# Performance work log

Measured on AMD Instinct MI355X. Metric: run time of the kernel, lower is better.

The kernel has to match this reference:

```python
import jax, jax.numpy as jnp
import numpy as np

B, NV, RN, SN = 1, 4, 1024, 128
H = W = 256
C_FEAT = 32   # img_feat_dim
D_VIEW = 32   # view transformer d_model
PE_D = 8      # PE_d_hid
D_RAY = D_VIEW + PE_D  # 40
NHEAD = 8
EPS_LN = 1e-5


def _layernorm(x, g, b):
    m = x.mean(-1, keepdims=True)
    v = ((x - m) ** 2).mean(-1, keepdims=True)
    return (x - m) * jax.lax.rsqrt(v + EPS_LN) * g + b


def _linear_attention(q, k, v):
    # LoFTR kernelized linear attention; q,k,v: (n, L, h, d)
    Q = jax.nn.elu(q) + 1.0
    K = jax.nn.elu(k) + 1.0
    L = v.shape[1]
    KV = jnp.einsum('nshd,nshv->nhdv', K, v / L)
    Z = 1.0 / (jnp.einsum('nlhd,nhd->nlh', Q, K.sum(axis=1)) + 1e-6)
    return jnp.einsum('nlhd,nhdv,nlh->nlhv', Q, KV, Z) * L


def _loftr_self_layer(x, Wq, Wk, Wv, Wm, g1, b1, W1, W2, g2, b2):
    # LoFTREncoderLayer with self-attention (x is both query and source)
    n, L, d = x.shape
    dim = d // NHEAD
    q = (x @ Wq).reshape(n, L, NHEAD, dim)
    k = (x @ Wk).reshape(n, L, NHEAD, dim)
    v = (x @ Wv).reshape(n, L, NHEAD, dim)
    msg = _linear_attention(q, k, v).reshape(n, L, d) @ Wm
    msg = _layernorm(msg, g1, b1)
    msg = jax.nn.relu(jnp.concatenate([x, msg], -1) @ W1) @ W2
    msg = _layernorm(msg, g2, b2)
    return x + msg


def _grid_sample_2d(img, pix):
    # img: (N,C,H,W); pix: (N,RN,SN,2) in pixel coords.
    # bilinear, align_corners=True, zero padding; mask = in-bounds.
    N, C, Hh, Ww = img.shape
    x, y = pix[..., 0], pix[..., 1]
    mask = ((x >= 0) & (x <= Ww - 1) & (y >= 0) & (y <= Hh - 1)).astype(img.dtype)
    x0 = jnp.floor(x)
    y0 = jnp.floor(y)
    flat = img.reshape(N, C, Hh * Ww)

    def gather(ix, iy):
        valid = ((ix >= 0) & (ix < Ww) & (iy >= 0) & (iy < Hh)).astype(img.dtype)
        idx = (jnp.clip(iy, 0, Hh - 1) * Ww + jnp.clip(ix, 0, Ww - 1)).astype(jnp.int32)
        out = jnp.take_along_axis(flat, idx.reshape(N, 1, -1), axis=2)
        return out.reshape(N, C, ix.shape[1], ix.shape[2]) * valid[:, None]

    wx1 = x - x0
    wy1 = y - y0
    out = (gather(x0, y0) * ((1 - wx1) * (1 - wy1))[:, None]
           + gather(x0 + 1, y0) * (wx1 * (1 - wy1))[:, None]
           + gather(x0, y0 + 1) * ((1 - wx1) * wy1)[:, None]
           + gather(x0 + 1, y0 + 1) * (wx1 * wy1)[:, None])
    return out, mask


def _order_posenc(d_hid, n):
    pos = np.arange(n)[:, None].astype(np.float64)
    j = np.arange(d_hid)[None, :]
    tab = pos / np.power(10000.0, 2 * (j // 2) / d_hid)
    tab[:, 0::2] = np.sin(tab[:, 0::2])
    tab[:, 1::2] = np.cos(tab[:, 1::2])
    return jnp.asarray(tab, dtype=jnp.float32)


def _forward(point3D, source_imgs, source_imgs_feat, ref_pose_inv, source_poses_inv,
             source_poses, view_token,
             vt_Wq, vt_Wk, vt_Wv, vt_Wm, vt_g1, vt_b1, vt_W1, vt_W2, vt_g2, vt_b2,
             rt_Wq, rt_Wk, rt_Wv, rt_Wm, rt_g1, rt_b1, rt_W1, rt_W2, rt_g2, rt_b2,
             dm_W1, dm_b1, dm_W2, dm_b2, dm_W3, dm_b3,
             rw_W1, rw_b1, rw_W2, rw_b2, rw_W3, rw_b3):
    b, nv, _, h, w = source_imgs.shape
    _, rn, sn, _ = point3D.shape

    # relative viewing directions (B,NV,RN,SN,3)
    v1 = point3D - ref_pose_inv[:, None, None, :3, -1]
    v2 = point3D[:, None] - source_poses_inv[:, :, None, None, :3, -1]
    v1 = v1 / jnp.linalg.norm(v1, axis=-1, keepdims=True)
    v2 = v2 / jnp.linalg.norm(v2, axis=-1, keepdims=True)
    dir_relative = v1[:, None] - v2

    # project points into all source views: (B,NV,3,RN,SN)
    pts_h = jnp.concatenate([point3D, jnp.ones_like(point3D[..., :1])], -1)
    pip = jnp.einsum('bnij,brsj->bnirs', source_poses, pts_h)[:, :, :3]
    mask_valid_depth = (pip[:, :, 2] > 0).astype(point3D.dtype)
    pix = pip[:, :, :2] / pip[:, :, 2:3]
    grid = jnp.moveaxis(pix, 2, -1).reshape(b * nv, rn, sn, 2)

    feat_s, mask = _grid_sample_2d(source_imgs_feat.reshape(b * nv, -1, h, w), grid)
    rgb_s, _ = _grid_sample_2d(source_imgs.reshape(b * nv, -1, h, w), grid)
    mask = mask.reshape(b, nv, rn, sn) * mask_valid_depth

    # per-point multi-view tokens: (B*RN*SN, NV, C)
    x = feat_s.reshape(b, nv, -1, rn, sn).transpose(0, 3, 4, 1, 2).reshape(b * rn * sn, nv, -1)
    tok = jnp.broadcast_to(view_token, (x.shape[0], 1, view_token.shape[-1]))
    x = jnp.concatenate([tok, x], axis=1)  # prepend view token -> L = NV+1
    x = _loftr_self_layer(x, vt_Wq, vt_Wk, vt_Wv, vt_Wm, vt_g1, vt_b1, vt_W1, vt_W2, vt_g2, vt_b2)

    x1 = jnp.moveaxis(x, 1, 0)          # (NV+1, B*RN*SN, C)
    view_feature = x1[1:]
    x = x1[0].reshape(b * rn, sn, -1)   # token output per sample along ray

    pe = _order_posenc(PE_D, sn)        # (SN, 8)
    x = jnp.concatenate([x, jnp.broadcast_to(pe, (b * rn, sn, PE_D))], -1)
    x = _loftr_self_layer(x, rt_Wq, rt_Wk, rt_Wv, rt_Wm, rt_g1, rt_b1, rt_W1, rt_W2, rt_g2, rt_b2)

    hdm = jax.nn.relu(x @ dm_W1 + dm_b1)
    hdm = jax.nn.relu(hdm @ dm_W2 + dm_b2)
    srdf = hdm @ dm_W3 + dm_b3           # (B*RN, SN, 1)

    # radiance blending weights over views
    vf = view_feature.reshape(nv, b, rn, sn, -1).transpose(1, 2, 3, 0, 4)  # (B,RN,SN,NV,C)
    dr = dir_relative.transpose(0, 2, 3, 1, 4)                             # (B,RN,SN,NV,3)
    xw = jnp.concatenate([vf, dr], -1)
    xw = jax.nn.relu(xw @ rw_W1 + rw_b1)
    xw = jax.nn.relu(xw @ rw_W2 + rw_b2)
    xw = xw @ rw_W3 + rw_b3                                                # (B,RN,SN,NV,1)
    m = mask.transpose(0, 2, 3, 1)[..., None]
    xw = jnp.where(m == 0, -1e9, xw)
    weight = jax.nn.softmax(xw, axis=-2)
    w_bn = weight[..., 0].transpose(0, 3, 1, 2)[:, :, None]                # (B,NV,1,RN,SN)
    radiance = (rgb_s.reshape(b, nv, 3, rn, sn) * w_bn).sum(axis=1)        # (B,3,RN,SN)
    radiance = radiance.transpose(0, 2, 3, 1).reshape(b * rn * sn, 3)
    return radiance, srdf, pip


def setup_inputs() -> dict:
    key = jax.random.key(0)
    ks = jax.random.split(key, 4)
    u = jax.random.uniform(ks[0], (B, RN, SN, 3), dtype=jnp.float32)
    point3D = jnp.concatenate([u[..., :2] - 0.5, u[..., 2:] + 1.0], -1)  # x,y in [-.5,.5], z in [1,2]
    source_imgs = jax.random.normal(ks[1], (B, NV, 3, H, W), dtype=jnp.float32) * 0.5
    source_imgs_feat = jax.random.normal(ks[2], (B, NV, C_FEAT, H, W), dtype=jnp.float32) * 0.5

    f = 200.0
    P = np.array([[f, 0, W / 2, 0], [0, f, H / 2, 0], [0, 0, 1, 0], [0, 0, 0, 1]], np.float32)
    source_poses = jnp.asarray(np.broadcast_to(P, (B, NV, 4, 4)).copy())
    ref_pose_inv = jnp.asarray(np.broadcast_to(np.eye(4, dtype=np.float32), (B, 4, 4)).copy())
    spi = np.broadcast_to(np.eye(4, dtype=np.float32), (B, NV, 4, 4)).copy()
    spi[:, :, 0, 3] = np.linspace(-0.2, 0.2, NV, dtype=np.float32)  # camera centers
    source_poses_inv = jnp.asarray(spi)

    pk = jax.random.split(ks[3], 20)

    def lin(k, i, o):
        return jax.random.normal(k, (i, o), dtype=jnp.float32) * 0.05

    d, dr = D_VIEW, D_RAY
    params = dict(
        view_token=jax.random.normal(pk[0], (1, d), dtype=jnp.float32),
        vt_Wq=lin(pk[1], d, d), vt_Wk=lin(pk[2], d, d), vt_Wv=lin(pk[3], d, d), vt_Wm=lin(pk[4], d, d),
        vt_g1=jnp.ones(d), vt_b1=jnp.zeros(d),
        vt_W1=lin(pk[5], 2 * d, 2 * d), vt_W2=lin(pk[6], 2 * d, d),
        vt_g2=jnp.ones(d), vt_b2=jnp.zeros(d),
        rt_Wq=lin(pk[7], dr, dr), rt_Wk=lin(pk[8], dr, dr), rt_Wv=lin(pk[9], dr, dr), rt_Wm=lin(pk[10], dr, dr),
        rt_g1=jnp.ones(dr), rt_b1=jnp.zeros(dr),
        rt_W1=lin(pk[11], 2 * dr, 2 * dr), rt_W2=lin(pk[12], 2 * dr, dr),
        rt_g2=jnp.ones(dr), rt_b2=jnp.zeros(dr),
        dm_W1=lin(pk[13], dr, 32), dm_b1=jnp.zeros(32),
        dm_W2=lin(pk[14], 32, 16), dm_b2=jnp.zeros(16),
        dm_W3=lin(pk[15], 16, 1), dm_b3=jnp.zeros(1),
        rw_W1=lin(pk[16], d + 3, 16), rw_b1=jnp.zeros(16),
        rw_W2=lin(pk[17], 16, 8), rw_b2=jnp.zeros(8),
        rw_W3=lin(pk[18], 8, 1), rw_b3=jnp.zeros(1),
    )
    out = dict(point3D=point3D, source_imgs=source_imgs, source_imgs_feat=source_imgs_feat,
               ref_pose_inv=ref_pose_inv, source_poses_inv=source_poses_inv,
               source_poses=source_poses)
    out.update(params)
    return out


def reference(point3D, source_imgs, source_imgs_feat, ref_pose_inv, source_poses_inv,
              source_poses, view_token,
              vt_Wq, vt_Wk, vt_Wv, vt_Wm, vt_g1, vt_b1, vt_W1, vt_W2, vt_g2, vt_b2,
              rt_Wq, rt_Wk, rt_Wv, rt_Wm, rt_g1, rt_b1, rt_W1, rt_W2, rt_g2, rt_b2,
              dm_W1, dm_b1, dm_W2, dm_b2, dm_W3, dm_b3,
              rw_W1, rw_b1, rw_W2, rw_b2, rw_W3, rw_b3):
    return _forward(point3D, source_imgs, source_imgs_feat, ref_pose_inv, source_poses_inv,
                    source_poses, view_token,
                    vt_Wq, vt_Wk, vt_Wv, vt_Wm, vt_g1, vt_b1, vt_W1, vt_W2, vt_g2, vt_b2,
                    rt_Wq, rt_Wk, rt_Wv, rt_Wm, rt_g1, rt_b1, rt_W1, rt_W2, rt_g2, rt_b2,
                    dm_W1, dm_b1, dm_W2, dm_b2, dm_W3, dm_b3,
                    rw_W1, rw_b1, rw_W2, rw_b2, rw_W3, rw_b3)
```

## Files before the change

### kernel.cpp

```cpp
#include <hip/hip_runtime.h>
#include <math.h>

#define NPTS   131072
#define NVIEW  4
#define IMH    256
#define IMW    256

#define WS_FEATT   0u
#define WS_IMGT    8388608u
#define WS_X1      9437184u
#define WS_XR      26214400u
#define WS_MSG     31457280u
#define WS_RGB     36700160u
#define WS_DIR     38273024u
#define WS_MASK    39845888u

__device__ __forceinline__ float elup1(float t) { return t > 0.f ? t + 1.f : expf(t); }

__global__ __launch_bounds__(256) void k0_transpose(
    const float* __restrict__ feat, const float* __restrict__ img,
    float* __restrict__ featT, float* __restrict__ imgT)
{
    int tid = blockIdx.x * 256 + threadIdx.x;
    int v = tid >> 16, pix = tid & 65535;
    float buf[32];
#pragma unroll
    for (int c = 0; c < 32; ++c)
        buf[c] = feat[((size_t)(v * 32 + c) << 16) + pix];
    float4* dst = (float4*)(featT + ((size_t)tid << 5));
#pragma unroll
    for (int q = 0; q < 8; ++q)
        dst[q] = make_float4(buf[4*q], buf[4*q+1], buf[4*q+2], buf[4*q+3]);
    float4 rgb;
    rgb.x = img[((size_t)(v * 3 + 0) << 16) + pix];
    rgb.y = img[((size_t)(v * 3 + 1) << 16) + pix];
    rgb.z = img[((size_t)(v * 3 + 2) << 16) + pix];
    rgb.w = 0.f;
    *(float4*)(imgT + ((size_t)tid << 2)) = rgb;
}

__global__ __launch_bounds__(256) void k1_geom_sample(
    const float* __restrict__ p3d, const float* __restrict__ rpi,
    const float* __restrict__ spi, const float* __restrict__ sp,
    const float* __restrict__ featT, const float* __restrict__ imgT,
    float* __restrict__ x1, float* __restrict__ rgbw,
    float* __restrict__ dirw, float* __restrict__ maskw,
    float* __restrict__ outpip)
{
    int tid = blockIdx.x * 256 + threadIdx.x;
    int p = tid >> 2, v = tid & 3;
    float X = p3d[p * 3 + 0], Y = p3d[p * 3 + 1], Z = p3d[p * 3 + 2];

    float a0 = X - rpi[3], a1 = Y - rpi[7], a2 = Z - rpi[11];
    float na = sqrtf(a0 * a0 + a1 * a1 + a2 * a2);
    a0 /= na; a1 /= na; a2 /= na;
    const float* sv = spi + v * 16;
    float b0 = X - sv[3], b1 = Y - sv[7], b2 = Z - sv[11];
    float nb = sqrtf(b0 * b0 + b1 * b1 + b2 * b2);
    b0 /= nb; b1 /= nb; b2 /= nb;
    dirw[(size_t)p * 12 + v * 3 + 0] = a0 - b0;
    dirw[(size_t)p * 12 + v * 3 + 1] = a1 - b1;
    dirw[(size_t)p * 12 + v * 3 + 2] = a2 - b2;

    const float* P = sp + v * 16;
    float pip0 = P[0] * X + P[1] * Y + P[2]  * Z + P[3];
    float pip1 = P[4] * X + P[5] * Y + P[6]  * Z + P[7];
    float pip2 = P[8] * X + P[9] * Y + P[10] * Z + P[11];
    outpip[(size_t)(v * 3 + 0) * NPTS + p] = pip0;
    outpip[(size_t)(v * 3 + 1) * NPTS + p] = pip1;
    outpip[(size_t)(v * 3 + 2) * NPTS + p] = pip2;

    float gx = pip0 / pip2, gy = pip1 / pip2;
    float inb = (gx >= 0.f && gx <= 255.f && gy >= 0.f && gy <= 255.f) ? 1.f : 0.f;
    float mvd = pip2 > 0.f ? 1.f : 0.f;
    maskw[(size_t)p * 4 + v] = inb * mvd;

    float x0f = floorf(gx), y0f = floorf(gy);
    float wx = gx - x0f, wy = gy - y0f;
    int ix0 = (int)x0f, iy0 = (int)y0f;
    float tw[4] = { (1.f-wx)*(1.f-wy), wx*(1.f-wy), (1.f-wx)*wy, wx*wy };
    int tdx[4] = { 0, 1, 0, 1 };
    int tdy[4] = { 0, 0, 1, 1 };

    float facc[32];
#pragma unroll
    for (int c = 0; c < 32; ++c) facc[c] = 0.f;
    float r0 = 0.f, r1 = 0.f, r2 = 0.f;

#pragma unroll
    for (int tno = 0; tno < 4; ++tno) {
        int ix = ix0 + tdx[tno], iy = iy0 + tdy[tno];
        float valid = (ix >= 0 && ix < IMW && iy >= 0 && iy < IMH) ? 1.f : 0.f;
        int cx = min(max(ix, 0), IMW - 1), cy = min(max(iy, 0), IMH - 1);
        float wgt = tw[tno] * valid;
        size_t base = ((size_t)v << 16) + ((size_t)cy << 8) + (size_t)cx;
        const float4* fp = (const float4*)(featT + base * 32);
#pragma unroll
        for (int q = 0; q < 8; ++q) {
            float4 f4 = fp[q];
            facc[4*q+0] += f4.x * wgt; facc[4*q+1] += f4.y * wgt;
            facc[4*q+2] += f4.z * wgt; facc[4*q+3] += f4.w * wgt;
        }
        float4 rp = *(const float4*)(imgT + base * 4);
        r0 += rp.x * wgt; r1 += rp.y * wgt; r2 += rp.z * wgt;
    }

    float4* xd = (float4*)(x1 + ((size_t)p * 4 + v) * 32);
#pragma unroll
    for (int q = 0; q < 8; ++q)
        xd[q] = make_float4(facc[4*q], facc[4*q+1], facc[4*q+2], facc[4*q+3]);
    rgbw[(size_t)p * 12 + v * 3 + 0] = r0;
    rgbw[(size_t)p * 12 + v * 3 + 1] = r1;
    rgbw[(size_t)p * 12 + v * 3 + 2] = r2;
}

#define K2_BLK    128
#define K2_PTS    24
#define K2_GRID   512
#define K2_NGRP   ((NPTS + K2_PTS - 1) / K2_PTS)

#define WQo   0
#define WKo   1024
#define WVo   2048
#define WMo   3072
#define W1o   4096
#define W2o   8192
#define LNo   10240

__device__ __forceinline__ void fma4(const float4 xv, const float* __restrict__ w,
                                     const int stride, float* __restrict__ acc)
{
#pragma unroll
    for (int j = 0; j < 32; ++j) acc[j] = fmaf(xv.x, w[j],            acc[j]);
#pragma unroll
    for (int j = 0; j < 32; ++j) acc[j] = fmaf(xv.y, w[stride + j],   acc[j]);
#pragma unroll
    for (int j = 0; j < 32; ++j) acc[j] = fmaf(xv.z, w[2*stride + j], acc[j]);
#pragma unroll
    for (int j = 0; j < 32; ++j) acc[j] = fmaf(xv.w, w[3*stride + j], acc[j]);
}

__global__ __launch_bounds__(K2_BLK) void k2_loftr1(
    float* __restrict__ x1g, const float* __restrict__ vtok,
    const float* __restrict__ Wq, const float* __restrict__ Wk,
    const float* __restrict__ Wv, const float* __restrict__ Wm,
    const float* __restrict__ g1v, const float* __restrict__ b1v,
    const float* __restrict__ W1, const float* __restrict__ W2,
    const float* __restrict__ g2v, const float* __restrict__ b2v,
    float* __restrict__ xr)
{
    __shared__ float wsm[10368];
    __shared__ float shr[8192];

    int t = threadIdx.x;
    for (int i = t; i < 1024; i += K2_BLK) {
        wsm[WQo + i] = Wq[i]; wsm[WKo + i] = Wk[i];
        wsm[WVo + i] = Wv[i]; wsm[WMo + i] = Wm[i];
    }
    for (int i = t; i < 4096; i += K2_BLK) wsm[W1o + i] = W1[i];
    for (int i = t; i < 2048; i += K2_BLK) wsm[W2o + i] = W2[i];
    if (t < 32) {
        wsm[LNo + t] = g1v[t]; wsm[LNo + 32 + t] = b1v[t];
        wsm[LNo + 64 + t] = g2v[t]; wsm[LNo + 96 + t] = b2v[t];
    }
    __syncthreads();

    int pl = t / 5, l = t - pl * 5;
    bool act = (t < K2_PTS * 5);
    if (!act) { pl = 0; l = 0; }
    const int rowbase = (pl * 5 + l) * 68;

    for (int grp = blockIdx.x; grp < K2_NGRP; grp += gridDim.x) {
        int p = grp * K2_PTS + pl;
        bool valid = act && (p < NPTS);
        int pload = p < NPTS ? p : NPTS - 1;
        const float4* xsrc = (l == 0) ? (const float4*)vtok
                                      : (const float4*)(x1g + ((size_t)pload * 4 + (l - 1)) * 32);

        __syncthreads();

        {
            float acc[32];
#pragma unroll
            for (int j = 0; j < 32; ++j) acc[j] = 0.f;
            for (int g = 0; g < 8; ++g) {
                float4 xv = xsrc[g];
                fma4(xv, &wsm[WKo + g * 128], 32, acc);
            }
            if (act) {
                float* krow = &shr[rowbase];
#pragma unroll
                for (int j = 0; j < 32; j += 4)
                    *(float4*)&krow[j] = make_float4(elup1(acc[j]), elup1(acc[j+1]),
                                                     elup1(acc[j+2]), elup1(acc[j+3]));
            }
        }
        {
            float acc[32];
#pragma unroll
            for (int j = 0; j < 32; ++j) acc[j] = 0.f;
            for (int g = 0; g < 8; ++g) {
                float4 xv = xsrc[g];
                fma4(xv, &wsm[WVo + g * 128], 32, acc);
            }
            if (act) {
                float* vrow = &shr[rowbase + 32];
#pragma unroll
                for (int j = 0; j < 32; j += 4)
                    *(float4*)&vrow[j] = make_float4(acc[j], acc[j+1], acc[j+2], acc[j+3]);
            }
        }
        __syncthreads();

        float macc[32];
#pragma unroll
        for (int j = 0; j < 32; ++j) macc[j] = 0.f;
        for (int h = 0; h < 8; ++h) {
            float q0 = 0.f, q1 = 0.f, q2 = 0.f, q3 = 0.f;
            for (int g = 0; g < 8; ++g) {
                float4 xv = xsrc[g];
                const float* w = &wsm[WQo + g * 128 + h * 4];
                q0 = fmaf(xv.x, w[0],  q0); q1 = fmaf(xv.x, w[1],  q1);
                q2 = fmaf(xv.x, w[2],  q2); q3 = fmaf(xv.x, w[3],  q3);
                q0 = fmaf(xv.y, w[32], q0); q1 = fmaf(xv.y, w[33], q1);
                q2 = fmaf(xv.y, w[34], q2); q3 = fmaf(xv.y, w[35], q3);
                q0 = fmaf(xv.z, w[64], q0); q1 = fmaf(xv.z, w[65], q1);
                q2 = fmaf(xv.z, w[66], q2); q3 = fmaf(xv.z, w[67], q3);
                q0 = fmaf(xv.w, w[96], q0); q1 = fmaf(xv.w, w[97], q1);
                q2 = fmaf(xv.w, w[98], q2); q3 = fmaf(xv.w, w[99], q3);
            }
            q0 = elup1(q0); q1 = elup1(q1); q2 = elup1(q2); q3 = elup1(q3);

            float kvm[16] = {0,0,0,0,0,0,0,0,0,0,0,0,0,0,0,0};
            float ks0 = 0.f, ks1 = 0.f, ks2 = 0.f, ks3 = 0.f;
#pragma unroll
            for (int l2 = 0; l2 < 5; ++l2) {
                const float* row = &shr[(pl * 5 + l2) * 68 + h * 4];
                float4 K4 = *(const float4*)row;
                float4 V4 = *(const float4*)(row + 32);
                kvm[0]  = fmaf(K4.x, V4.x, kvm[0]);  kvm[1]  = fmaf(K4.x, V4.y, kvm[1]);
                kvm[2]  = fmaf(K4.x, V4.z, kvm[2]);  kvm[3]  = fmaf(K4.x, V4.w, kvm[3]);
                kvm[4]  = fmaf(K4.y, V4.x, kvm[4]);  kvm[5]  = fmaf(K4.y, V4.y, kvm[5]);
                kvm[6]  = fmaf(K4.y, V4.z, kvm[6]);  kvm[7]  = fmaf(K4.y, V4.w, kvm[7]);
                kvm[8]  = fmaf(K4.z, V4.x, kvm[8]);  kvm[9]  = fmaf(K4.z, V4.y, kvm[9]);
                kvm[10] = fmaf(K4.z, V4.z, kvm[10]); kvm[11] = fmaf(K4.z, V4.w, kvm[11]);
                kvm[12] = fmaf(K4.w, V4.x, kvm[12]); kvm[13] = fmaf(K4.w, V4.y, kvm[13]);
                kvm[14] = fmaf(K4.w, V4.z, kvm[14]); kvm[15] = fmaf(K4.w, V4.w, kvm[15]);
                ks0 += K4.x; ks1 += K4.y; ks2 += K4.z; ks3 += K4.w;
            }
            float den = 1e-6f + q0*ks0 + q1*ks1 + q2*ks2 + q3*ks3;
            float inv = 1.f / den;
            float o0 = (q0*kvm[0] + q1*kvm[4] + q2*kvm[8]  + q3*kvm[12]) * inv;
            float o1 = (q0*kvm[1] + q1*kvm[5] + q2*kvm[9]  + q3*kvm[13]) * inv;
            float o2 = (q0*kvm[2] + q1*kvm[6] + q2*kvm[10] + q3*kvm[14]) * inv;
            float o3 = (q0*kvm[3] + q1*kvm[7] + q2*kvm[11] + q3*kvm[15]) * inv;

            const float* wm = &wsm[WMo + h * 4 * 32];
#pragma unroll
            for (int j = 0; j < 32; ++j) macc[j] = fmaf(o0, wm[j],      macc[j]);
#pragma unroll
            for (int j = 0; j < 32; ++j) macc[j] = fmaf(o1, wm[32 + j], macc[j]);
#pragma unroll
            for (int j = 0; j < 32; ++j) macc[j] = fmaf(o2, wm[64 + j], macc[j]);
#pragma unroll
            for (int j = 0; j < 32; ++j) macc[j] = fmaf(o3, wm[96 + j], macc[j]);
        }

        float msg[32];
        {
            float s1 = 0.f, s2 = 0.f;
#pragma unroll
            for (int j = 0; j < 32; ++j) { s1 += macc[j]; s2 += macc[j] * macc[j]; }
            float m  = s1 * (1.f / 32.f);
            float va = s2 * (1.f / 32.f) - m * m;
            float rs = rsqrtf(va + 1e-5f);
#pragma unroll
            for (int j = 0; j < 32; ++j)
                msg[j] = (macc[j] - m) * rs * wsm[LNo + j] + wsm[LNo + 32 + j];
        }
        __syncthreads();

#pragma unroll
        for (int g = 0; g < 8; ++g)
            *(float4*)&shr[(g * K2_BLK + t) * 4] =
                make_float4(msg[4*g], msg[4*g+1], msg[4*g+2], msg[4*g+3]);

        float oacc[32];
#pragma unroll
        for (int j = 0; j < 32; ++j) oacc[j] = 0.f;
        for (int half = 0; half < 2; ++half) {
            const int j0 = half * 32;
            float hacc[32];
#pragma unroll
            for (int j = 0; j < 32; ++j) hacc[j] = 0.f;
            for (int g = 0; g < 8; ++g) {
                float4 xv = xsrc[g];
                fma4(xv, &wsm[W1o + (g * 4) * 64 + j0], 64, hacc);
            }
            for (int g = 0; g < 8; ++g) {
                float4 mv = *(const float4*)&shr[(g * K2_BLK + t) * 4];
                fma4(mv, &wsm[W1o + (32 + g * 4) * 64 + j0], 64, hacc);
            }
#pragma unroll
            for (int j = 0; j < 32; j += 4)
                *(float4*)&shr[4096 + ((j >> 2) * K2_BLK + t) * 4] =
                    make_float4(fmaxf(hacc[j], 0.f),   fmaxf(hacc[j+1], 0.f),
                                fmaxf(hacc[j+2], 0.f), fmaxf(hacc[j+3], 0.f));
            for (int g = 0; g < 8; ++g) {
                float4 hv = *(const float4*)&shr[4096 + (g * K2_BLK + t) * 4];
                fma4(hv, &wsm[W2o + (j0 + g * 4) * 32], 32, oacc);
            }
        }

        {
            float s1 = 0.f, s2 = 0.f;
#pragma unroll
            for (int j = 0; j < 32; ++j) { s1 += oacc[j]; s2 += oacc[j] * oacc[j]; }
            float m  = s1 * (1.f / 32.f);
            float va = s2 * (1.f / 32.f) - m * m;
            float rs = rsqrtf(va + 1e-5f);

            if (valid) {
                float y[32];
#pragma unroll
                for (int g = 0; g < 8; ++g) {
                    float4 x4 = xsrc[g];
                    y[4*g] = x4.x; y[4*g+1] = x4.y; y[4*g+2] = x4.z; y[4*g+3] = x4.w;
                }
#pragma unroll
                for (int j = 0; j < 32; ++j)
                    y[j] += (oacc[j] - m) * rs * wsm[LNo + 64 + j] + wsm[LNo + 96 + j];

                if (l == 0) {
                    float4* dst = (float4*)(xr + (size_t)p * 40);
#pragma unroll
                    for (int g = 0; g < 8; ++g)
                        dst[g] = make_float4(y[4*g], y[4*g+1], y[4*g+2], y[4*g+3]);
                    int sidx = p & 127;
#pragma unroll
                    for (int c = 0; c < 8; ++c) {
                        float den = (c < 2) ? 1.f : (c < 4) ? 10.f : (c < 6) ? 100.f : 1000.f;
                        float arg = (float)sidx / den;
                        xr[(size_t)p * 40 + 32 + c] = (c & 1) ? cosf(arg) : sinf(arg);
                    }
                } else {
                    float4* dst = (float4*)(x1g + ((size_t)p * 4 + (l - 1)) * 32);
#pragma unroll
                    for (int g = 0; g < 8; ++g)
                        dst[g] = make_float4(y[4*g], y[4*g+1], y[4*g+2], y[4*g+3]);
                }
            }
        }
    }
}

__global__ __launch_bounds__(320) void k3a_attn(
    const float* __restrict__ xr,
    const float* __restrict__ Wq, const float* __restrict__ Wk,
    const float* __restrict__ Wv, const float* __restrict__ Wm,
    const float* __restrict__ g1, const float* __restrict__ b1,
    float* __restrict__ msg)
{
    __shared__ float kb[5120];
    __shared__ float vb[5120];
    __shared__ float wb[1600];
    __shared__ float kvb[200];
    __shared__ float ksb[40];
    int t = threadIdx.x, r = blockIdx.x;
    const float* xbase = xr + (size_t)r * 5120;
    int lg = t / 40, c = t % 40;

    for (int i = t; i < 1600; i += 320) wb[i] = Wk[i];
    __syncthreads();
    {
        float acc[16];
#pragma unroll
        for (int i = 0; i < 16; ++i) acc[i] = 0.f;
        for (int kk = 0; kk < 40; ++kk) {
            float w = wb[kk * 40 + c];
#pragma unroll
            for (int i = 0; i < 16; ++i) acc[i] += xbase[(lg * 16 + i) * 40 + kk] * w;
        }
#pragma unroll
        for (int i = 0; i < 16; ++i) kb[(lg * 16 + i) * 40 + c] = elup1(acc[i]);
    }
    __syncthreads();
    for (int i = t; i < 1600; i += 320) wb[i] = Wv[i];
    __syncthreads();
    {
        float acc[16];
#pragma unroll
        for (int i = 0; i < 16; ++i) acc[i] = 0.f;
        for (int kk = 0; kk < 40; ++kk) {
            float w = wb[kk * 40 + c];
#pragma unroll
            for (int i = 0; i < 16; ++i) acc[i] += xbase[(lg * 16 + i) * 40 + kk] * w;
        }
#pragma unroll
        for (int i = 0; i < 16; ++i) vb[(lg * 16 + i) * 40 + c] = acc[i];
    }
    __syncthreads();
    if (t < 200) {
        int h = t / 25, e = (t / 5) % 5, d = t % 5;
        float kv = 0.f, ks = 0.f;
        for (int s2 = 0; s2 < 128; ++s2) {
            float kvv = kb[s2 * 40 + h * 5 + e];
            float vv  = vb[s2 * 40 + h * 5 + d];
            kv += kvv * vv; ks += kvv;
        }
        kvb[t] = kv;
        if (d == 0) ksb[h * 5 + e] = ks;
    }
    __syncthreads();
    for (int i = t; i < 1600; i += 320) wb[i] = Wq[i];
    __syncthreads();
    {
        float acc[16];
#pragma unroll
        for (int i = 0; i < 16; ++i) acc[i] = 0.f;
        for (int kk = 0; kk < 40; ++kk) {
            float w = wb[kk * 40 + c];
#pragma unroll
            for (int i = 0; i < 16; ++i) acc[i] += xbase[(lg * 16 + i) * 40 + kk] * w;
        }
#pragma unroll
        for (int i = 0; i < 16; ++i) kb[(lg * 16 + i) * 40 + c] = elup1(acc[i]);
    }
    __syncthreads();
    {
        int h = c / 5, d = c % 5;
#pragma unroll 4
        for (int i = 0; i < 16; ++i) {
            int l = lg * 16 + i;
            float den = 1e-6f, o = 0.f;
#pragma unroll
            for (int e = 0; e < 5; ++e) {
                float q = kb[l * 40 + h * 5 + e];
                den += q * ksb[h * 5 + e];
                o   += q * kvb[h * 25 + e * 5 + d];
            }
            vb[l * 40 + c] = o / den;
        }
    }
    __syncthreads();
    for (int i = t; i < 1600; i += 320) wb[i] = Wm[i];
    __syncthreads();
    {
        float acc[16];
#pragma unroll
        for (int i = 0; i < 16; ++i) acc[i] = 0.f;
        for (int kk = 0; kk < 40; ++kk) {
            float w = wb[kk * 40 + c];
#pragma unroll
            for (int i = 0; i < 16; ++i) acc[i] += vb[(lg * 16 + i) * 40 + kk] * w;
        }
#pragma unroll
        for (int i = 0; i < 16; ++i) kb[(lg * 16 + i) * 40 + c] = acc[i];
    }
    __syncthreads();
    if (t < 128) {
        float s1 = 0.f, s2v = 0.f;
        for (int j = 0; j < 40; ++j) { float x = kb[t * 40 + j]; s1 += x; s2v += x * x; }
        float m = s1 * (1.f / 40.f), va = s2v * (1.f / 40.f) - m * m;
        float rs = rsqrtf(va + 1e-5f);
        for (int j = 0; j < 40; ++j)
            msg[((size_t)r * 128 + t) * 40 + j] = (kb[t * 40 + j] - m) * rs * g1[j] + b1[j];
    }
}

__global__ __launch_bounds__(320) void k3b_ffn(
    float* __restrict__ xr, const float* __restrict__ msg,
    const float* __restrict__ W1, const float* __restrict__ W2,
    const float* __restrict__ g2, const float* __restrict__ b2)
{
    __shared__ float hb[10240];
    __shared__ float wb[3200];
    int t = threadIdx.x, r = blockIdx.x;
    int lg = t / 40, c = t % 40;
    const float* xbase = xr + (size_t)r * 5120;
    const float* mbase = msg + (size_t)r * 5120;

    float hA[16], hB[16];
#pragma unroll
    for (int i = 0; i < 16; ++i) { hA[i] = 0.f; hB[i] = 0.f; }

    for (int i = t; i < 3200; i += 320) wb[i] = W1[i];
    __syncthreads();
    for (int kk = 0; kk < 40; ++kk) {
        float wa = wb[kk * 80 + c], wbb = wb[kk * 80 + c + 40];
#pragma unroll
        for (int i = 0; i < 16; ++i) {
            float xv = xbase[(lg * 16 + i) * 40 + kk];
            hA[i] += xv * wa; hB[i] += xv * wbb;
        }
    }
    __syncthreads();
    for (int i = t; i < 3200; i += 320) wb[i] = W1[3200 + i];
    __syncthreads();
    for (int kk = 0; kk < 40; ++kk) {
        float wa = wb[kk * 80 + c], wbb = wb[kk * 80 + c + 40];
#pragma unroll
        for (int i = 0; i < 16; ++i) {
            float mv = mbase[(lg * 16 + i) * 40 + kk];
            hA[i] += mv * wa; hB[i] += mv * wbb;
        }
    }
#pragma unroll
    for (int i = 0; i < 16; ++i) {
        hb[(lg * 16 + i) * 80 + c]      = fmaxf(hA[i], 0.f);
        hb[(lg * 16 + i) * 80 + c + 40] = fmaxf(hB[i], 0.f);
    }
    __syncthreads();
    for (int i = t; i < 3200; i += 320) wb[i] = W2[i];
    __syncthreads();
    float oa[16];
#pragma unroll
    for (int i = 0; i < 16; ++i) oa[i] = 0.f;
    for (int kk = 0; kk < 80; ++kk) {
        float w = wb[kk * 40 + c];
#pragma unroll
        for (int i = 0; i < 16; ++i) oa[i] += hb[(lg * 16 + i) * 80 + kk] * w;
    }
    __syncthreads();
#pragma unroll
    for (int i = 0; i < 16; ++i) hb[(lg * 16 + i) * 40 + c] = oa[i];
    __syncthreads();
    if (t < 128) {
        float s1 = 0.f, s2v = 0.f;
        for (int j = 0; j < 40; ++j) { float x = hb[t * 40 + j]; s1 += x; s2v += x * x; }
        float m = s1 * (1.f / 40.f), va = s2v * (1.f / 40.f) - m * m;
        float rs = rsqrtf(va + 1e-5f);
        for (int j = 0; j < 40; ++j) {
            float y = xbase[t * 40 + j] + (hb[t * 40 + j] - m) * rs * g2[j] + b2[j];
            xr[(size_t)r * 5120 + t * 40 + j] = y;
        }
    }
}

__global__ __launch_bounds__(256) void k4_dm(
    const float* __restrict__ xr,
    const float* __restrict__ W1, const float* __restrict__ b1,
    const float* __restrict__ W2, const float* __restrict__ b2,
    const float* __restrict__ W3, const float* __restrict__ b3,
    float* __restrict__ out1)
{
    __shared__ float s[1857];
    int t = threadIdx.x;
    for (int i = t; i < 1280; i += 256) s[i] = W1[i];
    if (t < 32) s[1280 + t] = b1[t];
    for (int i = t; i < 512; i += 256) s[1312 + i] = W2[i];
    if (t < 16) { s[1824 + t] = b2[t]; s[1840 + t] = W3[t]; }
    if (t == 0) s[1856] = b3[0];
    __syncthreads();

    int p = blockIdx.x * 256 + t;
    float x[40];
    const float4* xp = (const float4*)(xr + (size_t)p * 40);
#pragma unroll
    for (int i = 0; i < 10; ++i) {
        float4 v4 = xp[i];
        x[4*i] = v4.x; x[4*i+1] = v4.y; x[4*i+2] = v4.z; x[4*i+3] = v4.w;
    }
    float h1[32];
#pragma unroll
    for (int j = 0; j < 32; ++j) h1[j] = s[1280 + j];
    for (int k = 0; k < 40; ++k) {
        float xv = x[k];
#pragma unroll
        for (int j = 0; j < 32; ++j) h1[j] += xv * s[k * 32 + j];
    }
#pragma unroll
    for (int j = 0; j < 32; ++j) h1[j] = fmaxf(h1[j], 0.f);
    float h2[16];
#pragma unroll
    for (int j = 0; j < 16; ++j) h2[j] = s[1824 + j];
    for (int k = 0; k < 32; ++k) {
        float hv = h1[k];
#pragma unroll
        for (int j = 0; j < 16; ++j) h2[j] += hv * s[1312 + k * 16 + j];
    }
    float o = s[1856];
#pragma unroll
    for (int j = 0; j < 16; ++j) o += fmaxf(h2[j], 0.f) * s[1840 + j];
    out1[p] = o;
}

__global__ __launch_bounds__(256) void k5_rw(
    const float* __restrict__ vf, const float* __restrict__ dirw,
    const float* __restrict__ maskw, const float* __restrict__ rgbw,
    const float* __restrict__ W1, const float* __restrict__ b1,
    const float* __restrict__ W2, const float* __restrict__ b2,
    const float* __restrict__ W3, const float* __restrict__ b3,
    float* __restrict__ out0)
{
    __shared__ float s[721];
    int t = threadIdx.x;
    for (int i = t; i < 560; i += 256) s[i] = W1[i];
    if (t < 16) s[560 + t] = b1[t];
    if (t < 128) s[576 + t] = W2[t];
    if (t < 8) { s[704 + t] = b2[t]; s[712 + t] = W3[t]; }
    if (t == 0) s[720] = b3[0];
    __syncthreads();

    int p = blockIdx.x * 256 + t;
    float xw[4];
#pragma unroll
    for (int v = 0; v < 4; ++v) {
        float in[35];
        const float4* vp = (const float4*)(vf + ((size_t)p * 4 + v) * 32);
#pragma unroll
        for (int q = 0; q < 8; ++q) {
            float4 f4 = vp[q];
            in[4*q] = f4.x; in[4*q+1] = f4.y; in[4*q+2] = f4.z; in[4*q+3] = f4.w;
        }
        in[32] = dirw[(size_t)p * 12 + v * 3 + 0];
        in[33] = dirw[(size_t)p * 12 + v * 3 + 1];
        in[34] = dirw[(size_t)p * 12 + v * 3 + 2];
        float h1[16];
#pragma unroll
        for (int j = 0; j < 16; ++j) h1[j] = s[560 + j];
        for (int k = 0; k < 35; ++k) {
            float xv = in[k];
#pragma unroll
            for (int j = 0; j < 16; ++j) h1[j] += xv * s[k * 16 + j];
        }
        float h2[8];
#pragma unroll
        for (int j = 0; j < 8; ++j) h2[j] = s[704 + j];
        for (int k = 0; k < 16; ++k) {
            float hv = fmaxf(h1[k], 0.f);
#pragma unroll
            for (int j = 0; j < 8; ++j) h2[j] += hv * s[576 + k * 8 + j];
        }
        float o = s[720];
#pragma unroll
        for (int j = 0; j < 8; ++j) o += fmaxf(h2[j], 0.f) * s[712 + j];
        xw[v] = (maskw[(size_t)p * 4 + v] == 0.f) ? -1e9f : o;
    }
    float m = fmaxf(fmaxf(xw[0], xw[1]), fmaxf(xw[2], xw[3]));
    float e0 = expf(xw[0] - m), e1 = expf(xw[1] - m), e2 = expf(xw[2] - m), e3 = expf(xw[3] - m);
    float inv = 1.f / (e0 + e1 + e2 + e3);
    float w4[4] = { e0 * inv, e1 * inv, e2 * inv, e3 * inv };
    float r0 = 0.f, r1 = 0.f, r2 = 0.f;
#pragma unroll
    for (int v = 0; v < 4; ++v) {
        r0 += rgbw[(size_t)p * 12 + v * 3 + 0] * w4[v];
        r1 += rgbw[(size_t)p * 12 + v * 3 + 1] * w4[v];
        r2 += rgbw[(size_t)p * 12 + v * 3 + 2] * w4[v];
    }
    out0[(size_t)p * 3 + 0] = r0;
    out0[(size_t)p * 3 + 1] = r1;
    out0[(size_t)p * 3 + 2] = r2;
}

extern "C" void kernel_launch(void* const* d_in, const int* in_sizes, int n_in,
                              void* d_out, int out_size, void* d_ws, size_t ws_size,
                              hipStream_t stream) {
    (void)in_sizes; (void)n_in; (void)out_size; (void)ws_size;
    const float* p3d   = (const float*)d_in[0];
    const float* imgs  = (const float*)d_in[1];
    const float* feat  = (const float*)d_in[2];
    const float* rpi   = (const float*)d_in[3];
    const float* spi   = (const float*)d_in[4];
    const float* sp    = (const float*)d_in[5];
    const float* vtok  = (const float*)d_in[6];
    const float* vtWq  = (const float*)d_in[7];
    const float* vtWk  = (const float*)d_in[8];
    const float* vtWv  = (const float*)d_in[9];
    const float* vtWm  = (const float*)d_in[10];
    const float* vtg1  = (const float*)d_in[11];
    const float* vtb1  = (const float*)d_in[12];
    const float* vtW1  = (const float*)d_in[13];
    const float* vtW2  = (const float*)d_in[14];
    const float* vtg2  = (const float*)d_in[15];
    const float* vtb2  = (const float*)d_in[16];
    const float* rtWq  = (const float*)d_in[17];
    const float* rtWk  = (const float*)d_in[18];
    const float* rtWv  = (const float*)d_in[19];
    const float* rtWm  = (const float*)d_in[20];
    const float* rtg1  = (const float*)d_in[21];
    const float* rtb1  = (const float*)d_in[22];
    const float* rtW1  = (const float*)d_in[23];
    const float* rtW2  = (const float*)d_in[24];
    const float* rtg2  = (const float*)d_in[25];
    const float* rtb2  = (const float*)d_in[26];
    const float* dmW1  = (const float*)d_in[27];
    const float* dmb1  = (const float*)d_in[28];
    const float* dmW2  = (const float*)d_in[29];
    const float* dmb2  = (const float*)d_in[30];
    const float* dmW3  = (const float*)d_in[31];
    const float* dmb3  = (const float*)d_in[32];
    const float* rwW1  = (const float*)d_in[33];
    const float* rwb1  = (const float*)d_in[34];
    const float* rwW2  = (const float*)d_in[35];
    const float* rwb2  = (const float*)d_in[36];
    const float* rwW3  = (const float*)d_in[37];
    const float* rwb3  = (const float*)d_in[38];

    float* out  = (float*)d_out;
    float* out0 = out;
    float* out1 = out + 393216;
    float* out2 = out + 524288;

    float* ws    = (float*)d_ws;
    float* featT = ws + WS_FEATT;
    float* imgT  = ws + WS_IMGT;
    float* x1    = ws + WS_X1;
    float* xr    = ws + WS_XR;
    float* msg   = ws + WS_MSG;
    float* rgbw  = ws + WS_RGB;
    float* dirw  = ws + WS_DIR;
    float* maskw = ws + WS_MASK;

    k0_transpose<<<dim3(1024), dim3(256), 0, stream>>>(feat, imgs, featT, imgT);
    k1_geom_sample<<<dim3(2048), dim3(256), 0, stream>>>(p3d, rpi, spi, sp, featT, imgT,
                                                         x1, rgbw, dirw, maskw, out2);
    k2_loftr1<<<dim3(K2_GRID), dim3(K2_BLK), 0, stream>>>(x1, vtok, vtWq, vtWk, vtWv, vtWm,
                                                    vtg1, vtb1, vtW1, vtW2, vtg2, vtb2, xr);
    k3a_attn<<<dim3(1024), dim3(320), 0, stream>>>(xr, rtWq, rtWk, rtWv, rtWm, rtg1, rtb1, msg);
    k3b_ffn<<<dim3(1024), dim3(320), 0, stream>>>(xr, msg, rtW1, rtW2, rtg2, rtb2);
    k4_dm<<<dim3(512), dim3(256), 0, stream>>>(xr, dmW1, dmb1, dmW2, dmb2, dmW3, dmb3, out1);
    k5_rw<<<dim3(512), dim3(256), 0, stream>>>(x1, dirw, maskw, rgbw,
                                               rwW1, rwb1, rwW2, rwb2, rwW3, rwb3, out0);
}
```

Baseline: 1.160 ms.

## Enlarge k2 LoFTR blocks, cache inputs in registers, drop shared-memory staging of MLP

The k2 view-transformer kernel now uses 512-thread blocks handling 88 points each instead of 128-thread blocks with 24 points, with a smaller persistent grid. Each thread loads its 32-float input row once into registers rather than re-reading it from global memory in every projection. The message and hidden activations of the feed-forward MLP stay in registers instead of going through shared memory, which removes a barrier and the LDS traffic. Inactive threads skip the compute entirely. In exchange, register pressure is much higher, which may cut occupancy or cause spills under the 512-thread launch bound.

After: 4.394 ms. 279% more time.

```diff
diff --git a/kernel.cpp b/kernel.cpp
--- a/kernel.cpp
+++ b/kernel.cpp
@@ -114,9 +114,10 @@
     rgbw[(size_t)p * 12 + v * 3 + 2] = r2;
 }
 
-#define K2_BLK    128
-#define K2_PTS    24
-#define K2_GRID   512
+#define K2_BLK    512
+#define K2_PTS    88
+#define K2_ROWS   (K2_PTS * 5)
+#define K2_GRID   256
 #define K2_NGRP   ((NPTS + K2_PTS - 1) / K2_PTS)
 
 #define WQo   0
@@ -150,7 +151,7 @@
     float* __restrict__ xr)
 {
     __shared__ float wsm[10368];
-    __shared__ float shr[8192];
+    __shared__ float shr[K2_ROWS * 68];
 
     int t = threadIdx.x;
     for (int i = t; i < 1024; i += K2_BLK) {
@@ -165,9 +166,9 @@
     }
     __syncthreads();
 
-    int pl = t / 5, l = t - pl * 5;
-    bool act = (t < K2_PTS * 5);
-    if (!act) { pl = 0; l = 0; }
+    bool act = (t < K2_ROWS);
+    int pl = act ? t / 5 : 0;
+    int l  = act ? t - pl * 5 : 0;
     const int rowbase = (pl * 5 + l) * 68;
 
     for (int grp = blockIdx.x; grp < K2_NGRP; grp += gridDim.x) {
@@ -176,34 +177,33 @@
         int pload = p < NPTS ? p : NPTS - 1;
         const float4* xsrc = (l == 0) ? (const float4*)vtok
                                       : (const float4*)(x1g + ((size_t)pload * 4 + (l - 1)) * 32);
+        float4 xv[8];
+#pragma unroll
+        for (int g = 0; g < 8; ++g) xv[g] = xsrc[g];
 
         __syncthreads();
 
-        {
-            float acc[32];
-#pragma unroll
-            for (int j = 0; j < 32; ++j) acc[j] = 0.f;
-            for (int g = 0; g < 8; ++g) {
-                float4 xv = xsrc[g];
-                fma4(xv, &wsm[WKo + g * 128], 32, acc);
-            }
-            if (act) {
+        if (act) {
+            {
+                float acc[32];
+#pragma unroll
+                for (int j = 0; j < 32; ++j) acc[j] = 0.f;
+#pragma unroll
+                for (int g = 0; g < 8; ++g)
+                    fma4(xv[g], &wsm[WKo + g * 128], 32, acc);
                 float* krow = &shr[rowbase];
 #pragma unroll
                 for (int j = 0; j < 32; j += 4)
                     *(float4*)&krow[j] = make_float4(elup1(acc[j]), elup1(acc[j+1]),
                                                      elup1(acc[j+2]), elup1(acc[j+3]));
             }
-        }
-        {
-            float acc[32];
-#pragma unroll
-            for (int j = 0; j < 32; ++j) acc[j] = 0.f;
-            for (int g = 0; g < 8; ++g) {
-                float4 xv = xsrc[g];
-                fma4(xv, &wsm[WVo + g * 128], 32, acc);
-            }
-            if (act) {
+            {
+                float acc[32];
+#pragma unroll
+                for (int j = 0; j < 32; ++j) acc[j] = 0.f;
+#pragma unroll
+                for (int g = 0; g < 8; ++g)
+                    fma4(xv[g], &wsm[WVo + g * 128], 32, acc);
                 float* vrow = &shr[rowbase + 32];
 #pragma unroll
                 for (int j = 0; j < 32; j += 4)
@@ -212,142 +212,137 @@
         }
         __syncthreads();
 
-        float macc[32];
-#pragma unroll
-        for (int j = 0; j < 32; ++j) macc[j] = 0.f;
-        for (int h = 0; h < 8; ++h) {
-            float q0 = 0.f, q1 = 0.f, q2 = 0.f, q3 = 0.f;
-            for (int g = 0; g < 8; ++g) {
-                float4 xv = xsrc[g];
-                const float* w = &wsm[WQo + g * 128 + h * 4];
-                q0 = fmaf(xv.x, w[0],  q0); q1 = fmaf(xv.x, w[1],  q1);
-                q2 = fmaf(xv.x, w[2],  q2); q3 = fmaf(xv.x, w[3],  q3);
-                q0 = fmaf(xv.y, w[32], q0); q1 = fmaf(xv.y, w[33], q1);
-                q2 = fmaf(xv.y, w[34], q2); q3 = fmaf(xv.y, w[35], q3);
-                q0 = fmaf(xv.z, w[64], q0); q1 = fmaf(xv.z, w[65], q1);
-                q2 = fmaf(xv.z, w[66], q2); q3 = fmaf(xv.z, w[67], q3);
-                q0 = fmaf(xv.w, w[96], q0); q1 = fmaf(xv.w, w[97], q1);
-                q2 = fmaf(xv.w, w[98], q2); q3 = fmaf(xv.w, w[99], q3);
+        if (act) {
+            float macc[32];
+#pragma unroll
+            for (int j = 0; j < 32; ++j) macc[j] = 0.f;
+            for (int h = 0; h < 8; ++h) {
+                float q0 = 0.f, q1 = 0.f, q2 = 0.f, q3 = 0.f;
+#pragma unroll
+                for (int g = 0; g < 8; ++g) {
+                    float4 v4 = xv[g];
+                    const float* w = &wsm[WQo + g * 128 + h * 4];
+                    q0 = fmaf(v4.x, w[0],  q0); q1 = fmaf(v4.x, w[1],  q1);
+                    q2 = fmaf(v4.x, w[2],  q2); q3 = fmaf(v4.x, w[3],  q3);
+                    q0 = fmaf(v4.y, w[32], q0); q1 = fmaf(v4.y, w[33], q1);
+                    q2 = fmaf(v4.y, w[34], q2); q3 = fmaf(v4.y, w[35], q3);
+                    q0 = fmaf(v4.z, w[64], q0); q1 = fmaf(v4.z, w[65], q1);
+                    q2 = fmaf(v4.z, w[66], q2); q3 = fmaf(v4.z, w[67], q3);
+                    q0 = fmaf(v4.w, w[96], q0); q1 = fmaf(v4.w, w[97], q1);
+                    q2 = fmaf(v4.w, w[98], q2); q3 = fmaf(v4.w, w[99], q3);
+                }
+                q0 = elup1(q0); q1 = elup1(q1); q2 = elup1(q2); q3 = elup1(q3);
+
+                float kvm[16] = {0,0,0,0,0,0,0,0,0,0,0,0,0,0,0,0};
+                float ks0 = 0.f, ks1 = 0.f, ks2 = 0.f, ks3 = 0.f;
+#pragma unroll
+                for (int l2 = 0; l2 < 5; ++l2) {
+                    const float* row = &shr[(pl * 5 + l2) * 68 + h * 4];
+                    float4 K4 = *(const float4*)row;
+                    float4 V4 = *(const float4*)(row + 32);
+                    kvm[0]  = fmaf(K4.x, V4.x, kvm[0]);  kvm[1]  = fmaf(K4.x, V4.y, kvm[1]);
+                    kvm[2]  = fmaf(K4.x, V4.z, kvm[2]);  kvm[3]  = fmaf(K4.x, V4.w, kvm[3]);
+                    kvm[4]  = fmaf(K4.y, V4.x, kvm[4]);  kvm[5]  = fmaf(K4.y, V4.y, kvm[5]);
+                    kvm[6]  = fmaf(K4.y, V4.z, kvm[6]);  kvm[7]  = fmaf(K4.y, V4.w, kvm[7]);
+                    kvm[8]  = fmaf(K4.z, V4.x, kvm[8]);  kvm[9]  = fmaf(K4.z, V4.y, kvm[9]);
+                    kvm[10] = fmaf(K4.z, V4.z, kvm[10]); kvm[11] = fmaf(K4.z, V4.w, kvm[11]);
+                    kvm[12] = fmaf(K4.w, V4.x, kvm[12]); kvm[13] = fmaf(K4.w, V4.y, kvm[13]);
+                    kvm[14] = fmaf(K4.w, V4.z, kvm[14]); kvm[15] = fmaf(K4.w, V4.w, kvm[15]);
+                    ks0 += K4.x; ks1 += K4.y; ks2 += K4.z; ks3 += K4.w;
+                }
+                float den = 1e-6f + q0*ks0 + q1*ks1 + q2*ks2 + q3*ks3;
+                float inv = 1.f / den;
+                float o0 = (q0*kvm[0] + q1*kvm[4] + q2*kvm[8]  + q3*kvm[12]) * inv;
+                float o1 = (q0*kvm[1] + q1*kvm[5] + q2*kvm[9]  + q3*kvm[13]) * inv;
+                float o2 = (q0*kvm[2] + q1*kvm[6] + q2*kvm[10] + q3*kvm[14]) * inv;
+                float o3 = (q0*kvm[3] + q1*kvm[7] + q2*kvm[11] + q3*kvm[15]) * inv;
+
+                const float* wm = &wsm[WMo + h * 4 * 32];
+#pragma unroll
+                for (int j = 0; j < 32; ++j) macc[j] = fmaf(o0, wm[j],      macc[j]);
+#pragma unroll
+                for (int j = 0; j < 32; ++j) macc[j] = fmaf(o1, wm[32 + j], macc[j]);
+#pragma unroll
+                for (int j = 0; j < 32; ++j) macc[j] = fmaf(o2, wm[64 + j], macc[j]);
+#pragma unroll
+                for (int j = 0; j < 32; ++j) macc[j] = fmaf(o3, wm[96 + j], macc[j]);
             }
-            q0 = elup1(q0); q1 = elup1(q1); q2 = elup1(q2); q3 = elup1(q3);
-
-            float kvm[16] = {0,0,0,0,0,0,0,0,0,0,0,0,0,0,0,0};
-            float ks0 = 0.f, ks1 = 0.f, ks2 = 0.f, ks3 = 0.f;
-#pragma unroll
-            for (int l2 = 0; l2 < 5; ++l2) {
-                const float* row = &shr[(pl * 5 + l2) * 68 + h * 4];
-                float4 K4 = *(const float4*)row;
-                float4 V4 = *(const float4*)(row + 32);
-                kvm[0]  = fmaf(K4.x, V4.x, kvm[0]);  kvm[1]  = fmaf(K4.x, V4.y, kvm[1]);
-                kvm[2]  = fmaf(K4.x, V4.z, kvm[2]);  kvm[3]  = fmaf(K4.x, V4.w, kvm[3]);
-                kvm[4]  = fmaf(K4.y, V4.x, kvm[4]);  kvm[5]  = fmaf(K4.y, V4.y, kvm[5]);
-                kvm[6]  = fmaf(K4.y, V4.z, kvm[6]);  kvm[7]  = fmaf(K4.y, V4.w, kvm[7]);
-                kvm[8]  = fmaf(K4.z, V4.x, kvm[8]);  kvm[9]  = fmaf(K4.z, V4.y, kvm[9]);
-                kvm[10] = fmaf(K4.z, V4.z, kvm[10]); kvm[11] = fmaf(K4.z, V4.w, kvm[11]);
-                kvm[12] = fmaf(K4.w, V4.x, kvm[12]); kvm[13] = fmaf(K4.w, V4.y, kvm[13]);
-                kvm[14] = fmaf(K4.w, V4.z, kvm[14]); kvm[15] = fmaf(K4.w, V4.w, kvm[15]);
-                ks0 += K4.x; ks1 += K4.y; ks2 += K4.z; ks3 += K4.w;
+
+            {
+                float s1 = 0.f, s2 = 0.f;
+#pragma unroll
+                for (int j = 0; j < 32; ++j) { s1 += macc[j]; s2 += macc[j] * macc[j]; }
+                float m  = s1 * (1.f / 32.f);
+                float va = s2 * (1.f / 32.f) - m * m;
+                float rs = rsqrtf(va + 1e-5f);
+#pragma unroll
+                for (int j = 0; j < 32; ++j)
+                    macc[j] = (macc[j] - m) * rs * wsm[LNo + j] + wsm[LNo + 32 + j];
             }
-            float den = 1e-6f + q0*ks0 + q1*ks1 + q2*ks2 + q3*ks3;
-            float inv = 1.f / den;
-            float o0 = (q0*kvm[0] + q1*kvm[4] + q2*kvm[8]  + q3*kvm[12]) * inv;
-            float o1 = (q0*kvm[1] + q1*kvm[5] + q2*kvm[9]  + q3*kvm[13]) * inv;
-            float o2 = (q0*kvm[2] + q1*kvm[6] + q2*kvm[10] + q3*kvm[14]) * inv;
-            float o3 = (q0*kvm[3] + q1*kvm[7] + q2*kvm[11] + q3*kvm[15]) * inv;
-
-            const float* wm = &wsm[WMo + h * 4 * 32];
-#pragma unroll
-            for (int j = 0; j < 32; ++j) macc[j] = fmaf(o0, wm[j],      macc[j]);
-#pragma unroll
-            for (int j = 0; j < 32; ++j) macc[j] = fmaf(o1, wm[32 + j], macc[j]);
-#pragma unroll
-            for (int j = 0; j < 32; ++j) macc[j] = fmaf(o2, wm[64 + j], macc[j]);
-#pragma unroll
-            for (int j = 0; j < 32; ++j) macc[j] = fmaf(o3, wm[96 + j], macc[j]);
-        }
-
-        float msg[32];
-        {
-            float s1 = 0.f, s2 = 0.f;
-#pragma unroll
-            for (int j = 0; j < 32; ++j) { s1 += macc[j]; s2 += macc[j] * macc[j]; }
-            float m  = s1 * (1.f / 32.f);
-            float va = s2 * (1.f / 32.f) - m * m;
-            float rs = rsqrtf(va + 1e-5f);
-#pragma unroll
-            for (int j = 0; j < 32; ++j)
-                msg[j] = (macc[j] - m) * rs * wsm[LNo + j] + wsm[LNo + 32 + j];
-        }
-        __syncthreads();
-
-#pragma unroll
-        for (int g = 0; g < 8; ++g)
-            *(float4*)&shr[(g * K2_BLK + t) * 4] =
-                make_float4(msg[4*g], msg[4*g+1], msg[4*g+2], msg[4*g+3]);
-
-        float oacc[32];
-#pragma unroll
-        for (int j = 0; j < 32; ++j) oacc[j] = 0.f;
-        for (int half = 0; half < 2; ++half) {
-            const int j0 = half * 32;
-            float hacc[32];
-#pragma unroll
-            for (int j = 0; j < 32; ++j) hacc[j] = 0.f;
-            for (int g = 0; g < 8; ++g) {
-                float4 xv = xsrc[g];
-                fma4(xv, &wsm[W1o + (g * 4) * 64 + j0], 64, hacc);
+
+            float oacc[32];
+#pragma unroll
+            for (int j = 0; j < 32; ++j) oacc[j] = 0.f;
+#pragma unroll
+            for (int half = 0; half < 2; ++half) {
+                const int j0 = half * 32;
+                float hacc[32];
+#pragma unroll
+                for (int j = 0; j < 32; ++j) hacc[j] = 0.f;
+#pragma unroll
+                for (int g = 0; g < 8; ++g)
+                    fma4(xv[g], &wsm[W1o + (g * 4) * 64 + j0], 64, hacc);
+#pragma unroll
+                for (int g = 0; g < 8; ++g) {
+                    float4 mv = make_float4(macc[4*g], macc[4*g+1], macc[4*g+2], macc[4*g+3]);
+                    fma4(mv, &wsm[W1o + (32 + g * 4) * 64 + j0], 64, hacc);
+                }
+#pragma unroll
+                for (int j = 0; j < 32; ++j) hacc[j] = fmaxf(hacc[j], 0.f);
+#pragma unroll
+                for (int g = 0; g < 8; ++g) {
+                    float4 hv = make_float4(hacc[4*g], hacc[4*g+1], hacc[4*g+2], hacc[4*g+3]);
+                    fma4(hv, &wsm[W2o + (j0 + g * 4) * 32], 32, oacc);
+                }
             }
-            for (int g = 0; g < 8; ++g) {
-                float4 mv = *(const float4*)&shr[(g * K2_BLK + t) * 4];
-                fma4(mv, &wsm[W1o + (32 + g * 4) * 64 + j0], 64, hacc);
-            }
-#pragma unroll
-            for (int j = 0; j < 32; j += 4)
-                *(float4*)&shr[4096 + ((j >> 2) * K2_BLK + t) * 4] =
-                    make_float4(fmaxf(hacc[j], 0.f),   fmaxf(hacc[j+1], 0.f),
-                                fmaxf(hacc[j+2], 0.f), fmaxf(hacc[j+3], 0.f));
-            for (int g = 0; g < 8; ++g) {
-                float4 hv = *(const float4*)&shr[4096 + (g * K2_BLK + t) * 4];
-                fma4(hv, &wsm[W2o + (j0 + g * 4) * 32], 32, oacc);
-            }
-        }
-
-        {
-            float s1 = 0.f, s2 = 0.f;
-#pragma unroll
-            for (int j = 0; j < 32; ++j) { s1 += oacc[j]; s2 += oacc[j] * oacc[j]; }
-            float m  = s1 * (1.f / 32.f);
-            float va = s2 * (1.f / 32.f) - m * m;
-            float rs = rsqrtf(va + 1e-5f);
-
-            if (valid) {
-                float y[32];
-#pragma unroll
-                for (int g = 0; g < 8; ++g) {
-                    float4 x4 = xsrc[g];
-                    y[4*g] = x4.x; y[4*g+1] = x4.y; y[4*g+2] = x4.z; y[4*g+3] = x4.w;
-                }
-#pragma unroll
-                for (int j = 0; j < 32; ++j)
-                    y[j] += (oacc[j] - m) * rs * wsm[LNo + 64 + j] + wsm[LNo + 96 + j];
-
-                if (l == 0) {
-                    float4* dst = (float4*)(xr + (size_t)p * 40);
-#pragma unroll
-                    for (int g = 0; g < 8; ++g)
-                        dst[g] = make_float4(y[4*g], y[4*g+1], y[4*g+2], y[4*g+3]);
-                    int sidx = p & 127;
-#pragma unroll
-                    for (int c = 0; c < 8; ++c) {
-                        float den = (c < 2) ? 1.f : (c < 4) ? 10.f : (c < 6) ? 100.f : 1000.f;
-                        float arg = (float)sidx / den;
-                        xr[(size_t)p * 40 + 32 + c] = (c & 1) ? cosf(arg) : sinf(arg);
+
+            {
+                float s1 = 0.f, s2 = 0.f;
+#pragma unroll
+                for (int j = 0; j < 32; ++j) { s1 += oacc[j]; s2 += oacc[j] * oacc[j]; }
+                float m  = s1 * (1.f / 32.f);
+                float va = s2 * (1.f / 32.f) - m * m;
+                float rs = rsqrtf(va + 1e-5f);
+
+                if (valid) {
+                    float y[32];
+#pragma unroll
+                    for (int g = 0; g < 8; ++g) {
+                        y[4*g] = xv[g].x; y[4*g+1] = xv[g].y;
+                        y[4*g+2] = xv[g].z; y[4*g+3] = xv[g].w;
                     }
-                } else {
-                    float4* dst = (float4*)(x1g + ((size_t)p * 4 + (l - 1)) * 32);
-#pragma unroll
-                    for (int g = 0; g < 8; ++g)
-                        dst[g] = make_float4(y[4*g], y[4*g+1], y[4*g+2], y[4*g+3]);
+#pragma unroll
+                    for (int j = 0; j < 32; ++j)
+                        y[j] += (oacc[j] - m) * rs * wsm[LNo + 64 + j] + wsm[LNo + 96 + j];
+
+                    if (l == 0) {
+                        float4* dst = (float4*)(xr + (size_t)p * 40);
+#pragma unroll
+                        for (int g = 0; g < 8; ++g)
+                            dst[g] = make_float4(y[4*g], y[4*g+1], y[4*g+2], y[4*g+3]);
+                        int sidx = p & 127;
+#pragma unroll
+                        for (int c = 0; c < 8; ++c) {
+                            float den = (c < 2) ? 1.f : (c < 4) ? 10.f : (c < 6) ? 100.f : 1000.f;
+                            float arg = (float)sidx / den;
+                            xr[(size_t)p * 40 + 32 + c] = (c & 1) ? cosf(arg) : sinf(arg);
+                        }
+                    } else {
+                        float4* dst = (float4*)(x1g + ((size_t)p * 4 + (l - 1)) * 32);
+#pragma unroll
+                        for (int g = 0; g < 8; ++g)
+                            dst[g] = make_float4(y[4*g], y[4*g+1], y[4*g+2], y[4*g+3]);
+                    }
                 }
             }
         }
```
